# Kernel optimization log

Measured on AMD Instinct MI355X. Metric: run time of the kernel, lower is better.

Reference implementation:

```python
import math
import jax, jax.numpy as jnp
import numpy as np

C = 256
CQ = C // 8
B, H, W = 8, 64, 64


def setup_inputs() -> dict:
    key = jax.random.key(0)
    k1, k2, k3, k4 = jax.random.split(key, 4)
    x = jax.random.normal(k1, (B, C, H, W), dtype=jnp.float32)
    # 1x1 conv weights, bias=False -> plain [out, in] matrices
    wq = jax.random.normal(k2, (CQ, C), dtype=jnp.float32) * 0.02
    wk = jax.random.normal(k3, (CQ, C), dtype=jnp.float32) * 0.02
    wv = jax.random.normal(k4, (C, C), dtype=jnp.float32) * 0.02
    # gamma init is zeros in the torch module; use small nonzero so output depends on attention path
    gamma = jnp.ones((1,), dtype=jnp.float32) * 0.5
    return {"x": x, "wq": wq, "wk": wk, "wv": wv, "gamma": gamma}


def reference(x, wq, wk, wv, gamma):
    b, c, h, w = x.shape
    n = h * w
    xr = x.reshape(b, c, n)                       # [B, C, N]
    q = jnp.einsum('oc,bcn->bon', wq, xr)         # [B, Cq, N]
    k = jnp.einsum('oc,bcn->bon', wk, xr)         # [B, Cq, N]
    v = jnp.einsum('oc,bcn->bon', wv, xr)         # [B, C, N]
    # attn[b, i, j] = softmax_j( q[:, i] . k[:, j] / sqrt(Cq) )
    scores = jnp.einsum('bci,bcj->bij', q, k) / math.sqrt(q.shape[1])  # [B, N, N]
    attn = jax.nn.softmax(scores, axis=-1)
    # out[b, c, m] = sum_n v[b, c, n] * attn[b, m, n]
    out = jnp.einsum('bcn,bmn->bcm', v, attn).reshape(b, c, h, w)
    return gamma[0] * out + x
```

## Files before the change

kernel.cpp:

```cpp
#include <hip/hip_runtime.h>

#define B_ 8
#define C_ 256
#define CQ_ 32
#define N_ 4096

typedef __attribute__((ext_vector_type(8))) short short8;
typedef __attribute__((ext_vector_type(4))) float float4v;

#define QSCALE 0.2550599232f

#if __has_builtin(__builtin_amdgcn_exp2f)
#define EXP2F __builtin_amdgcn_exp2f
#else
#define EXP2F exp2f
#endif

static __device__ __forceinline__ unsigned short f2bf(float f) {
  unsigned int u = __float_as_uint(f);
  u += 0x7FFFu + ((u >> 16) & 1u);
  return (unsigned short)(u >> 16);
}

static __device__ __forceinline__ void async16(void* lds, const void* g) {
  __builtin_amdgcn_global_load_lds(
      (const __attribute__((address_space(1))) unsigned int*)g,
      (__attribute__((address_space(3))) unsigned int*)lds, 16, 0, 0);
}

__global__ __launch_bounds__(256) void wconv_kernel(
    const float* __restrict__ wq, const float* __restrict__ wk,
    const float* __restrict__ wv, unsigned short* __restrict__ w_bf) {
  int o = blockIdx.x * 8 + (threadIdx.x >> 5);
  int c8 = (threadIdx.x & 31) * 8;
  const float* src; float sc = 1.f;
  if (o < 32)      { src = wq + (size_t)o * 256; sc = QSCALE; }
  else if (o < 64) { src = wk + (size_t)(o - 32) * 256; }
  else             { src = wv + (size_t)(o - 64) * 256; }
  float4 a = *(const float4*)(src + c8);
  float4 bq = *(const float4*)(src + c8 + 4);
  unsigned short t[8] = {f2bf(a.x*sc), f2bf(a.y*sc), f2bf(a.z*sc), f2bf(a.w*sc),
                         f2bf(bq.x*sc), f2bf(bq.y*sc), f2bf(bq.z*sc), f2bf(bq.w*sc)};
  *(uint4*)(w_bf + (size_t)o * 256 + c8) = *(const uint4*)t;
}

__global__ __launch_bounds__(256, 2) void proj_kernel(
    const float* __restrict__ x, const unsigned short* __restrict__ w_bf,
    unsigned short* __restrict__ qT, unsigned short* __restrict__ kT,
    unsigned short* __restrict__ v) {
  __shared__ __align__(16) unsigned short xb[2][64 * 32];
  int tid = threadIdx.x, wave = tid >> 6, lane = tid & 63;
  int q16 = lane >> 4, l16 = lane & 15;
  int b = blockIdx.x, n0 = blockIdx.y * 64;

  int p = tid & 15, n4g = tid >> 4;
  const float* x0 = x + (size_t)b * C_ * N_ + n0 + n4g * 4;

  auto stage = [&](int buf, int ks) {
    const float* r0 = x0 + (size_t)(ks * 32 + 2 * p) * N_;
    float4 fa = *(const float4*)(r0);
    float4 fb = *(const float4*)(r0 + N_);
    float va[4] = {fa.x, fa.y, fa.z, fa.w};
    float vb[4] = {fb.x, fb.y, fb.z, fb.w};
    #pragma unroll
    for (int i = 0; i < 4; ++i) {
      int n = n4g * 4 + i;
      unsigned int pk = (unsigned int)f2bf(va[i]) | ((unsigned int)f2bf(vb[i]) << 16);
      int so = (p >> 2) ^ ((n >> 1) & 3);
      *(unsigned int*)(&xb[buf][n * 32 + so * 8 + (p & 3) * 2]) = pk;
    }
  };

  float4v acc[5][4];
  float4v zerov = {0.f, 0.f, 0.f, 0.f};
  #pragma unroll
  for (int mt = 0; mt < 5; ++mt)
    for (int nt = 0; nt < 4; ++nt) acc[mt][nt] = zerov;

  stage(0, 0);
  __syncthreads();

  int o0 = wave * 80;
  int sxo = (q16 ^ ((l16 >> 1) & 3)) * 8;
  #pragma unroll 1
  for (int ks = 0; ks < 8; ++ks) {
    if (ks < 7) stage((ks + 1) & 1, ks + 1);
    short8 af[5], bf4[4];
    #pragma unroll
    for (int mt = 0; mt < 5; ++mt)
      af[mt] = *(const short8*)(w_bf + (size_t)(o0 + mt * 16 + l16) * 256 + ks * 32 + q16 * 8);
    #pragma unroll
    for (int nt = 0; nt < 4; ++nt)
      bf4[nt] = *(const short8*)(&xb[ks & 1][(nt * 16 + l16) * 32 + sxo]);
    #pragma unroll
    for (int mt = 0; mt < 5; ++mt)
      #pragma unroll
      for (int nt = 0; nt < 4; ++nt)
        acc[mt][nt] = __builtin_amdgcn_mfma_f32_16x16x32_bf16(af[mt], bf4[nt], acc[mt][nt], 0, 0, 0);
    __syncthreads();
  }

  #pragma unroll
  for (int mt = 0; mt < 5; ++mt) {
    int og = o0 + mt * 16 + q16 * 4;
    #pragma unroll
    for (int nt = 0; nt < 4; ++nt) {
      int n = n0 + nt * 16 + l16;
      unsigned short t[4];
      if (og < 64) {
        #pragma unroll
        for (int r = 0; r < 4; ++r) t[r] = f2bf(acc[mt][nt][r]);
        unsigned short* dst = (og < 32) ? (qT + ((size_t)b * N_ + n) * CQ_ + og)
                                        : (kT + ((size_t)b * N_ + n) * CQ_ + (og - 32));
        *(uint2*)dst = *(const uint2*)t;
      } else {
        #pragma unroll
        for (int r = 0; r < 4; ++r)
          v[((size_t)b * C_ + og - 64 + r) * N_ + n] = f2bf(acc[mt][nt][r]);
      }
    }
  }
}

__global__ __launch_bounds__(512, 2) void attn_kernel(
    const unsigned short* __restrict__ qT, const unsigned short* __restrict__ kT,
    const unsigned short* __restrict__ v, const float* __restrict__ x,
    const float* __restrict__ gamma, float* __restrict__ out) {
  __shared__ __align__(16) unsigned short v_lds[256 * 64];
  __shared__ __align__(16) unsigned short kt_lds[2][64 * 32];
  __shared__ __align__(16) unsigned short p_lds[128 * 64];
  __shared__ float l_lds[128];

  int tid = threadIdx.x, wave = tid >> 6, lane = tid & 63;
  int q16 = lane >> 4, l16 = lane & 15;
  int bid = blockIdx.x, b = bid & 7, m0 = (bid >> 3) * 128;

  short8 qfrag = *(const short8*)(qT + ((size_t)b * N_ + m0 + wave * 16 + l16) * CQ_ + q16 * 8);

  const unsigned short* vbase = v + (size_t)b * C_ * N_;
  auto stageV = [&](int j0) {
    #pragma unroll
    for (int it = 0; it < 4; ++it) {
      int r = wave * 32 + it * 8 + (lane >> 3);
      int lo = (lane & 7) ^ (lane >> 3);
      async16(&v_lds[(wave * 32 + it * 8) * 64], vbase + (size_t)r * N_ + j0 + lo * 8);
    }
  };
  auto stageK = [&](int buf, int j0) {
    if (wave >= 4) {
      int w4 = wave - 4;
      int r = w4 * 16 + (lane >> 2);
      int lo = (lane & 3) ^ ((r >> 1) & 3);
      async16(&kt_lds[buf][w4 * 16 * 32], kT + ((size_t)b * N_ + j0 + r) * CQ_ + lo * 8);
    }
  };

  stageK(0, 0);
  stageV(0);
  __syncthreads();

  float4v acc[4][4];
  float4v zerov = {0.f, 0.f, 0.f, 0.f};
  #pragma unroll
  for (int mt = 0; mt < 4; ++mt)
    for (int ct = 0; ct < 4; ++ct) acc[mt][ct] = zerov;
  float lrun[4] = {0.f, 0.f, 0.f, 0.f};

  int kro = q16 ^ ((l16 >> 1) & 3);
  int vro = l16 & 7;
  int lo8 = l16 >> 3, li = l16 & 7;
  int h = wave >> 2, cq = wave & 3;

  for (int j = 0; j < 64; ++j) {
    int cur = j & 1;
    float4v s[4];
    #pragma unroll
    for (int jt = 0; jt < 4; ++jt) {
      short8 kf = *(const short8*)(&kt_lds[cur][(jt * 16 + l16) * 32 + kro * 8]);
      s[jt] = __builtin_amdgcn_mfma_f32_16x16x32_bf16(qfrag, kf, zerov, 0, 0, 0);
    }

    #pragma unroll
    for (int r = 0; r < 4; ++r) {
      float p0 = EXP2F(s[0][r]), p1 = EXP2F(s[1][r]);
      float p2 = EXP2F(s[2][r]), p3 = EXP2F(s[3][r]);
      lrun[r] += (p0 + p1) + (p2 + p3);
      int prow = wave * 16 + q16 * 4 + r;
      int rl = (q16 * 4 + r) & 7;
      unsigned short* pr = &p_lds[prow * 64 + li];
      int o0 = lo8 ^ rl;
      pr[(o0 ^ 0) * 8] = (unsigned short)(__float_as_uint(p0) >> 16);
      pr[(o0 ^ 2) * 8] = (unsigned short)(__float_as_uint(p1) >> 16);
      pr[(o0 ^ 4) * 8] = (unsigned short)(__float_as_uint(p2) >> 16);
      pr[(o0 ^ 6) * 8] = (unsigned short)(__float_as_uint(p3) >> 16);
    }
    if (j == 63) {
      #pragma unroll
      for (int r = 0; r < 4; ++r) {
        float t = lrun[r];
        t += __shfl_xor(t, 1); t += __shfl_xor(t, 2);
        t += __shfl_xor(t, 4); t += __shfl_xor(t, 8);
        if (l16 == 0) l_lds[wave * 16 + q16 * 4 + r] = t;
      }
    }
    __syncthreads();

    if (j < 63) stageK(cur ^ 1, (j + 1) * 64);

    #pragma unroll
    for (int ks = 0; ks < 2; ++ks) {
      short8 pf[4], vf[4];
      #pragma unroll
      for (int mt = 0; mt < 4; ++mt)
        pf[mt] = *(const short8*)(&p_lds[(h * 64 + mt * 16 + l16) * 64 + ((ks * 4 + q16) ^ vro) * 8]);
      #pragma unroll
      for (int ct = 0; ct < 4; ++ct)
        vf[ct] = *(const short8*)(&v_lds[(cq * 64 + ct * 16 + l16) * 64 + ((ks * 4 + q16) ^ vro) * 8]);
      #pragma unroll
      for (int mt = 0; mt < 4; ++mt)
        #pragma unroll
        for (int ct = 0; ct < 4; ++ct)
          acc[mt][ct] = __builtin_amdgcn_mfma_f32_16x16x32_bf16(pf[mt], vf[ct], acc[mt][ct], 0, 0, 0);
    }
    __syncthreads();

    if (j < 63) stageV((j + 1) * 64);
  }

  float g = gamma[0];
  #pragma unroll
  for (int mt = 0; mt < 4; ++mt) {
    float linv[4];
    #pragma unroll
    for (int r = 0; r < 4; ++r) linv[r] = 1.f / l_lds[h * 64 + mt * 16 + q16 * 4 + r];
    int n = m0 + h * 64 + mt * 16 + q16 * 4;
    #pragma unroll
    for (int ct = 0; ct < 4; ++ct) {
      int c = cq * 64 + ct * 16 + l16;
      size_t off = ((size_t)b * C_ + c) * N_ + n;
      float4 xv = *(const float4*)(x + off);
      float4 o;
      o.x = g * acc[mt][ct][0] * linv[0] + xv.x;
      o.y = g * acc[mt][ct][1] * linv[1] + xv.y;
      o.z = g * acc[mt][ct][2] * linv[2] + xv.z;
      o.w = g * acc[mt][ct][3] * linv[3] + xv.w;
      *(float4*)(out + off) = o;
    }
  }
}

extern "C" void kernel_launch(void* const* d_in, const int* in_sizes, int n_in,
                              void* d_out, int out_size, void* d_ws, size_t ws_size,
                              hipStream_t stream) {
  const float* x     = (const float*)d_in[0];
  const float* wq    = (const float*)d_in[1];
  const float* wk    = (const float*)d_in[2];
  const float* wv    = (const float*)d_in[3];
  const float* gamma = (const float*)d_in[4];
  float* out = (float*)d_out;

  unsigned short* qT  = (unsigned short*)d_ws;
  unsigned short* kT  = qT + (size_t)B_ * N_ * CQ_;
  unsigned short* vv  = kT + (size_t)B_ * N_ * CQ_;
  unsigned short* wbf = vv + (size_t)B_ * C_ * N_;

  hipLaunchKernelGGL(wconv_kernel, dim3(40), dim3(256), 0, stream, wq, wk, wv, wbf);
  hipLaunchKernelGGL(proj_kernel, dim3(8, 64), dim3(256), 0, stream, x, wbf, qT, kT, vv);
  hipLaunchKernelGGL(attn_kernel, dim3(256), dim3(512), 0, stream, qT, kT, vv, x, gamma, out);
}
```

Baseline: 191.6 us.

## Load K and V fragments directly from global into registers, halve attention block

The attention kernel no longer stages K and V tiles in LDS through async global-to-LDS copies. Each wave now reads its MFMA K and V fragments straight from global memory into registers, and only the P tile stays in LDS, double-buffered, so one barrier per iteration can go. Blocks shrink from 512 to 256 threads covering 64 query rows, and the grid doubles. In exchange, V is re-read from global or L2 by twice as many blocks, and the per-lane strided global loads may add latency that is no longer hidden by LDS staging.

```diff
diff --git a/kernel.cpp b/kernel.cpp
--- a/kernel.cpp
+++ b/kernel.cpp
@@ -20,12 +20,6 @@
   unsigned int u = __float_as_uint(f);
   u += 0x7FFFu + ((u >> 16) & 1u);
   return (unsigned short)(u >> 16);
-}
-
-static __device__ __forceinline__ void async16(void* lds, const void* g) {
-  __builtin_amdgcn_global_load_lds(
-      (const __attribute__((address_space(1))) unsigned int*)g,
-      (__attribute__((address_space(3))) unsigned int*)lds, 16, 0, 0);
 }
 
 __global__ __launch_bounds__(256) void wconv_kernel(
@@ -122,72 +116,56 @@
   }
 }
 
-__global__ __launch_bounds__(512, 2) void attn_kernel(
+__global__ __launch_bounds__(256, 2) void attn_kernel(
     const unsigned short* __restrict__ qT, const unsigned short* __restrict__ kT,
     const unsigned short* __restrict__ v, const float* __restrict__ x,
     const float* __restrict__ gamma, float* __restrict__ out) {
-  __shared__ __align__(16) unsigned short v_lds[256 * 64];
-  __shared__ __align__(16) unsigned short kt_lds[2][64 * 32];
-  __shared__ __align__(16) unsigned short p_lds[128 * 64];
-  __shared__ float l_lds[128];
+  __shared__ __align__(16) unsigned short p_lds[2][64 * 64];
+  __shared__ float l_lds[64];
 
   int tid = threadIdx.x, wave = tid >> 6, lane = tid & 63;
   int q16 = lane >> 4, l16 = lane & 15;
-  int bid = blockIdx.x, b = bid & 7, m0 = (bid >> 3) * 128;
+  int bid = blockIdx.x, b = bid & 7, m0 = (bid >> 3) * 64;
 
   short8 qfrag = *(const short8*)(qT + ((size_t)b * N_ + m0 + wave * 16 + l16) * CQ_ + q16 * 8);
 
-  const unsigned short* vbase = v + (size_t)b * C_ * N_;
-  auto stageV = [&](int j0) {
-    #pragma unroll
-    for (int it = 0; it < 4; ++it) {
-      int r = wave * 32 + it * 8 + (lane >> 3);
-      int lo = (lane & 7) ^ (lane >> 3);
-      async16(&v_lds[(wave * 32 + it * 8) * 64], vbase + (size_t)r * N_ + j0 + lo * 8);
-    }
-  };
-  auto stageK = [&](int buf, int j0) {
-    if (wave >= 4) {
-      int w4 = wave - 4;
-      int r = w4 * 16 + (lane >> 2);
-      int lo = (lane & 3) ^ ((r >> 1) & 3);
-      async16(&kt_lds[buf][w4 * 16 * 32], kT + ((size_t)b * N_ + j0 + r) * CQ_ + lo * 8);
-    }
-  };
-
-  stageK(0, 0);
-  stageV(0);
-  __syncthreads();
+  const unsigned short* kbase = kT + ((size_t)b * N_ + l16) * CQ_ + q16 * 8;
+  const unsigned short* vbase = v + ((size_t)b * C_ + wave * 64 + l16) * N_ + q16 * 8;
 
   float4v acc[4][4];
   float4v zerov = {0.f, 0.f, 0.f, 0.f};
   #pragma unroll
   for (int mt = 0; mt < 4; ++mt)
+    #pragma unroll
     for (int ct = 0; ct < 4; ++ct) acc[mt][ct] = zerov;
   float lrun[4] = {0.f, 0.f, 0.f, 0.f};
 
-  int kro = q16 ^ ((l16 >> 1) & 3);
+  int lo8 = l16 >> 3, li = l16 & 7;
   int vro = l16 & 7;
-  int lo8 = l16 >> 3, li = l16 & 7;
-  int h = wave >> 2, cq = wave & 3;
-
+
+  short8 kf[4];
+  #pragma unroll
+  for (int jt = 0; jt < 4; ++jt)
+    kf[jt] = *(const short8*)(kbase + (size_t)(jt * 16) * CQ_);
+
+  const unsigned short* vj = vbase;
+
+  #pragma unroll 1
   for (int j = 0; j < 64; ++j) {
-    int cur = j & 1;
+    unsigned short* pcur = p_lds[j & 1];
+
     float4v s[4];
     #pragma unroll
-    for (int jt = 0; jt < 4; ++jt) {
-      short8 kf = *(const short8*)(&kt_lds[cur][(jt * 16 + l16) * 32 + kro * 8]);
-      s[jt] = __builtin_amdgcn_mfma_f32_16x16x32_bf16(qfrag, kf, zerov, 0, 0, 0);
-    }
+    for (int jt = 0; jt < 4; ++jt)
+      s[jt] = __builtin_amdgcn_mfma_f32_16x16x32_bf16(qfrag, kf[jt], zerov, 0, 0, 0);
 
     #pragma unroll
     for (int r = 0; r < 4; ++r) {
       float p0 = EXP2F(s[0][r]), p1 = EXP2F(s[1][r]);
       float p2 = EXP2F(s[2][r]), p3 = EXP2F(s[3][r]);
       lrun[r] += (p0 + p1) + (p2 + p3);
-      int prow = wave * 16 + q16 * 4 + r;
       int rl = (q16 * 4 + r) & 7;
-      unsigned short* pr = &p_lds[prow * 64 + li];
+      unsigned short* pr = pcur + (wave * 16 + q16 * 4 + r) * 64 + li;
       int o0 = lo8 ^ rl;
       pr[(o0 ^ 0) * 8] = (unsigned short)(__float_as_uint(p0) >> 16);
       pr[(o0 ^ 2) * 8] = (unsigned short)(__float_as_uint(p1) >> 16);
@@ -205,26 +183,29 @@
     }
     __syncthreads();
 
-    if (j < 63) stageK(cur ^ 1, (j + 1) * 64);
+    if (j < 63) {
+      const unsigned short* kn = kbase + (size_t)((j + 1) * 64) * CQ_;
+      #pragma unroll
+      for (int jt = 0; jt < 4; ++jt)
+        kf[jt] = *(const short8*)(kn + (size_t)(jt * 16) * CQ_);
+    }
 
     #pragma unroll
     for (int ks = 0; ks < 2; ++ks) {
-      short8 pf[4], vf[4];
+      short8 vf[4], pf[4];
+      #pragma unroll
+      for (int ct = 0; ct < 4; ++ct)
+        vf[ct] = *(const short8*)(vj + (size_t)(ct * 16) * N_ + ks * 32);
       #pragma unroll
       for (int mt = 0; mt < 4; ++mt)
-        pf[mt] = *(const short8*)(&p_lds[(h * 64 + mt * 16 + l16) * 64 + ((ks * 4 + q16) ^ vro) * 8]);
-      #pragma unroll
-      for (int ct = 0; ct < 4; ++ct)
-        vf[ct] = *(const short8*)(&v_lds[(cq * 64 + ct * 16 + l16) * 64 + ((ks * 4 + q16) ^ vro) * 8]);
+        pf[mt] = *(const short8*)(pcur + (mt * 16 + l16) * 64 + ((ks * 4 + q16) ^ vro) * 8);
       #pragma unroll
       for (int mt = 0; mt < 4; ++mt)
         #pragma unroll
         for (int ct = 0; ct < 4; ++ct)
           acc[mt][ct] = __builtin_amdgcn_mfma_f32_16x16x32_bf16(pf[mt], vf[ct], acc[mt][ct], 0, 0, 0);
     }
-    __syncthreads();
-
-    if (j < 63) stageV((j + 1) * 64);
+    vj += 64;
   }
 
   float g = gamma[0];
@@ -232,11 +213,11 @@
   for (int mt = 0; mt < 4; ++mt) {
     float linv[4];
     #pragma unroll
-    for (int r = 0; r < 4; ++r) linv[r] = 1.f / l_lds[h * 64 + mt * 16 + q16 * 4 + r];
-    int n = m0 + h * 64 + mt * 16 + q16 * 4;
+    for (int r = 0; r < 4; ++r) linv[r] = 1.f / l_lds[mt * 16 + q16 * 4 + r];
+    int n = m0 + mt * 16 + q16 * 4;
     #pragma unroll
     for (int ct = 0; ct < 4; ++ct) {
-      int c = cq * 64 + ct * 16 + l16;
+      int c = wave * 64 + ct * 16 + l16;
       size_t off = ((size_t)b * C_ + c) * N_ + n;
       float4 xv = *(const float4*)(x + off);
       float4 o;
@@ -266,5 +247,5 @@
 
   hipLaunchKernelGGL(wconv_kernel, dim3(40), dim3(256), 0, stream, wq, wk, wv, wbf);
   hipLaunchKernelGGL(proj_kernel, dim3(8, 64), dim3(256), 0, stream, x, wbf, qT, kT, vv);
-  hipLaunchKernelGGL(attn_kernel, dim3(256), dim3(512), 0, stream, qT, kT, vv, x, gamma, out);
-}
+  hipLaunchKernelGGL(attn_kernel, dim3(512), dim3(256), 0, stream, qT, kT, vv, x, gamma, out);
+}
```

Result: slower. 258.6 us (+35.0%).

## Double-buffer V and P tiles, load K fragments into registers, drop a barrier

Applied to the files above, without the earlier changes.

V and P shared-memory tiles are double-buffered, so the next V tile is prefetched right after the first barrier and the trailing per-iteration __syncthreads is removed. K fragments are now read straight from global memory into registers for the next iteration instead of being staged through LDS. This cuts one barrier per iteration and overlaps V loads with the PV MFMAs. In exchange, LDS use per block rises to about 96KB, which likely prevents two 512-thread blocks from sharing a CU, and K global-load latency may land on the critical path.

```diff
diff --git a/kernel.cpp b/kernel.cpp
--- a/kernel.cpp
+++ b/kernel.cpp
@@ -126,9 +126,8 @@
     const unsigned short* __restrict__ qT, const unsigned short* __restrict__ kT,
     const unsigned short* __restrict__ v, const float* __restrict__ x,
     const float* __restrict__ gamma, float* __restrict__ out) {
-  __shared__ __align__(16) unsigned short v_lds[256 * 64];
-  __shared__ __align__(16) unsigned short kt_lds[2][64 * 32];
-  __shared__ __align__(16) unsigned short p_lds[128 * 64];
+  __shared__ __align__(16) unsigned short v_lds[2][256 * 64];
+  __shared__ __align__(16) unsigned short p_lds[2][128 * 64];
   __shared__ float l_lds[128];
 
   int tid = threadIdx.x, wave = tid >> 6, lane = tid & 63;
@@ -138,47 +137,45 @@
   short8 qfrag = *(const short8*)(qT + ((size_t)b * N_ + m0 + wave * 16 + l16) * CQ_ + q16 * 8);
 
   const unsigned short* vbase = v + (size_t)b * C_ * N_;
-  auto stageV = [&](int j0) {
+  auto stageV = [&](int buf, int j0) {
     #pragma unroll
     for (int it = 0; it < 4; ++it) {
       int r = wave * 32 + it * 8 + (lane >> 3);
       int lo = (lane & 7) ^ (lane >> 3);
-      async16(&v_lds[(wave * 32 + it * 8) * 64], vbase + (size_t)r * N_ + j0 + lo * 8);
+      async16(&v_lds[buf][(wave * 32 + it * 8) * 64], vbase + (size_t)r * N_ + j0 + lo * 8);
     }
   };
-  auto stageK = [&](int buf, int j0) {
-    if (wave >= 4) {
-      int w4 = wave - 4;
-      int r = w4 * 16 + (lane >> 2);
-      int lo = (lane & 3) ^ ((r >> 1) & 3);
-      async16(&kt_lds[buf][w4 * 16 * 32], kT + ((size_t)b * N_ + j0 + r) * CQ_ + lo * 8);
-    }
-  };
-
-  stageK(0, 0);
-  stageV(0);
+
+  const unsigned short* kbase = kT + ((size_t)b * N_ + l16) * CQ_ + q16 * 8;
+  short8 kreg[4];
+  #pragma unroll
+  for (int jt = 0; jt < 4; ++jt)
+    kreg[jt] = *(const short8*)(kbase + (size_t)(jt * 16) * CQ_);
+
+  stageV(0, 0);
   __syncthreads();
 
   float4v acc[4][4];
   float4v zerov = {0.f, 0.f, 0.f, 0.f};
   #pragma unroll
   for (int mt = 0; mt < 4; ++mt)
+    #pragma unroll
     for (int ct = 0; ct < 4; ++ct) acc[mt][ct] = zerov;
   float lrun[4] = {0.f, 0.f, 0.f, 0.f};
 
-  int kro = q16 ^ ((l16 >> 1) & 3);
+  int lo8 = l16 >> 3, li = l16 & 7;
   int vro = l16 & 7;
-  int lo8 = l16 >> 3, li = l16 & 7;
   int h = wave >> 2, cq = wave & 3;
 
+  #pragma unroll 1
   for (int j = 0; j < 64; ++j) {
     int cur = j & 1;
+    unsigned short* pcur = p_lds[cur];
+
     float4v s[4];
     #pragma unroll
-    for (int jt = 0; jt < 4; ++jt) {
-      short8 kf = *(const short8*)(&kt_lds[cur][(jt * 16 + l16) * 32 + kro * 8]);
-      s[jt] = __builtin_amdgcn_mfma_f32_16x16x32_bf16(qfrag, kf, zerov, 0, 0, 0);
-    }
+    for (int jt = 0; jt < 4; ++jt)
+      s[jt] = __builtin_amdgcn_mfma_f32_16x16x32_bf16(qfrag, kreg[jt], zerov, 0, 0, 0);
 
     #pragma unroll
     for (int r = 0; r < 4; ++r) {
@@ -187,7 +184,7 @@
       lrun[r] += (p0 + p1) + (p2 + p3);
       int prow = wave * 16 + q16 * 4 + r;
       int rl = (q16 * 4 + r) & 7;
-      unsigned short* pr = &p_lds[prow * 64 + li];
+      unsigned short* pr = pcur + prow * 64 + li;
       int o0 = lo8 ^ rl;
       pr[(o0 ^ 0) * 8] = (unsigned short)(__float_as_uint(p0) >> 16);
       pr[(o0 ^ 2) * 8] = (unsigned short)(__float_as_uint(p1) >> 16);
@@ -205,26 +202,29 @@
     }
     __syncthreads();
 
-    if (j < 63) stageK(cur ^ 1, (j + 1) * 64);
+    if (j < 63) {
+      stageV(cur ^ 1, (j + 1) * 64);
+      const unsigned short* kn = kbase + (size_t)((j + 1) * 64) * CQ_;
+      #pragma unroll
+      for (int jt = 0; jt < 4; ++jt)
+        kreg[jt] = *(const short8*)(kn + (size_t)(jt * 16) * CQ_);
+    }
 
     #pragma unroll
     for (int ks = 0; ks < 2; ++ks) {
       short8 pf[4], vf[4];
       #pragma unroll
       for (int mt = 0; mt < 4; ++mt)
-        pf[mt] = *(const short8*)(&p_lds[(h * 64 + mt * 16 + l16) * 64 + ((ks * 4 + q16) ^ vro) * 8]);
+        pf[mt] = *(const short8*)(pcur + (h * 64 + mt * 16 + l16) * 64 + ((ks * 4 + q16) ^ vro) * 8);
       #pragma unroll
       for (int ct = 0; ct < 4; ++ct)
-        vf[ct] = *(const short8*)(&v_lds[(cq * 64 + ct * 16 + l16) * 64 + ((ks * 4 + q16) ^ vro) * 8]);
+        vf[ct] = *(const short8*)(&v_lds[cur][(cq * 64 + ct * 16 + l16) * 64 + ((ks * 4 + q16) ^ vro) * 8]);
       #pragma unroll
       for (int mt = 0; mt < 4; ++mt)
         #pragma unroll
         for (int ct = 0; ct < 4; ++ct)
           acc[mt][ct] = __builtin_amdgcn_mfma_f32_16x16x32_bf16(pf[mt], vf[ct], acc[mt][ct], 0, 0, 0);
     }
-    __syncthreads();
-
-    if (j < 63) stageV((j + 1) * 64);
   }
 
   float g = gamma[0];
```

Result: slower. 218.3 us (+14.0%).
